# Performance work log

Hardware: AMD Instinct MI355X
Metric: run time of the kernel (lower is better)

The kernel has to match this reference:

```python
import jax, jax.numpy as jnp
import numpy as np

EPS = 1e-12

def _fuzzy_laplacian_weights(theta, src, dst, num_nodes):
    # Continuous edge directions: forward (src->dst) strength cos^2(theta),
    # backward (dst->src) strength sin^2(theta); each symmetrically normalized
    # by its own weighted in/out degrees.
    c = jnp.cos(theta); s = jnp.sin(theta)
    w_f = c * c
    w_b = s * s
    def norm(w):
        deg_out = jax.ops.segment_sum(w, src, num_segments=num_nodes)
        deg_in = jax.ops.segment_sum(w, dst, num_segments=num_nodes)
        return w * jax.lax.rsqrt(deg_out[src] * deg_in[dst] + EPS)
    return norm(w_f), norm(w_b)

def setup_inputs() -> dict:
    key = jax.random.key(0)
    ks = jax.random.split(key, 12)
    N, E, D, H, O, L = 50000, 800000, 128, 128, 64, 2
    x = jax.random.normal(ks[0], (N, D), dtype=jnp.float32)
    edge_index = jax.random.randint(ks[1], (2, E), 0, N, dtype=jnp.int64)
    theta = jax.random.uniform(ks[2], (E,), dtype=jnp.float32) * (np.pi / 2)
    sc = 0.05
    Ws2d = jax.random.normal(ks[3], (L, D, H), dtype=jnp.float32) * sc
    Wd2s = jax.random.normal(ks[4], (L, D, H), dtype=jnp.float32) * sc
    Wself = jax.random.normal(ks[5], (L, D, H), dtype=jnp.float32) * sc
    bs2d = jnp.zeros((L, H), jnp.float32)
    bd2s = jnp.zeros((L, H), jnp.float32)
    bself = jnp.zeros((L, H), jnp.float32)
    W_ro = jax.random.normal(ks[6], (H, O), dtype=jnp.float32) * sc
    b_ro = jnp.zeros((O,), jnp.float32)
    return {"x": x, "edge_index": edge_index, "theta": theta,
            "Ws2d": Ws2d, "Wd2s": Wd2s, "Wself": Wself,
            "bs2d": bs2d, "bd2s": bd2s, "bself": bself,
            "W_ro": W_ro, "b_ro": b_ro}

def reference(x, edge_index, theta, Ws2d, Wd2s, Wself, bs2d, bd2s, bself, W_ro, b_ro):
    N = x.shape[0]
    src, dst = edge_index[0], edge_index[1]
    w_f, w_b = _fuzzy_laplacian_weights(theta, src, dst, N)
    L = Ws2d.shape[0]
    for i in range(L):
        xj = x[src]                               # [E, D] gather
        a_s2d = jax.ops.segment_sum(xj * w_f[:, None], dst, num_segments=N)
        a_d2s = jax.ops.segment_sum(xj * w_b[:, None], dst, num_segments=N)
        h = (a_s2d @ Ws2d[i] + bs2d[i]
             + a_d2s @ Wd2s[i] + bd2s[i]
             + x @ Wself[i] + bself[i])
        if i != L - 1:
            h = jax.nn.relu(h)
            h = h / jnp.maximum(jnp.linalg.norm(h, axis=1, keepdims=True), EPS)
        x = h
    return x @ W_ro + b_ro
```

## Files before the change

kernel.cpp:

```cpp
#include <hip/hip_runtime.h>
#include <math.h>


constexpr int D = 128;
typedef unsigned long long u64;
typedef __attribute__((ext_vector_type(8))) short bf16x8;
typedef __attribute__((ext_vector_type(4))) float f32x4;

__device__ __forceinline__ u64 pack_wc(float f) {
    return (1ULL << 44) | (u64)(f * 16777216.0f + 0.5f);
}
__device__ __forceinline__ void unpack_wc(u64 p, float& sumf, float& cnt) {
    cnt  = (float)(unsigned)(p >> 44);
    sumf = (float)(p & ((1ULL << 44) - 1)) * (1.0f / 16777216.0f);
}

__device__ __forceinline__ void split_bf16(float x, short& hi, short& lo) {
    unsigned xb = __float_as_uint(x);
    hi = (short)(xb >> 16);
    float h = __uint_as_float(xb & 0xffff0000u);
    lo = (short)(__float_as_uint(x - h) >> 16);
}

__global__ __launch_bounds__(256) void edge_wdeg_kernel(
    const float* __restrict__ theta, const int* __restrict__ src, const int* __restrict__ dst,
    u64* __restrict__ packed_out, u64* __restrict__ packed_in, int E)
{
    int e = blockIdx.x * 256 + threadIdx.x;
    if (e >= E) return;
    float c = cosf(theta[e]);
    u64 p = pack_wc(c * c);
    atomicAdd(&packed_out[src[e]], p);
    atomicAdd(&packed_in[dst[e]], p);
}

__global__ __launch_bounds__(1024) void scan_kernel(
    const u64* __restrict__ packed_in, int* __restrict__ startv, int N)
{
    __shared__ int wsum[16];
    __shared__ int carry;
    if (threadIdx.x == 0) carry = 0;
    __syncthreads();
    const int lane = threadIdx.x & 63, wid = threadIdx.x >> 6;
    for (int base = 0; base < N; base += 2048) {
        int i0 = base + threadIdx.x * 2;
        int i1 = i0 + 1;
        int v0 = (i0 < N) ? (int)(packed_in[i0] >> 44) : 0;
        int v1 = (i1 < N) ? (int)(packed_in[i1] >> 44) : 0;
        int pair = v0 + v1;
        int x = pair;
        #pragma unroll
        for (int d = 1; d < 64; d <<= 1) {
            int t = __shfl_up(x, d);
            if (lane >= d) x += t;
        }
        if (lane == 63) wsum[wid] = x;
        __syncthreads();
        if (wid == 0) {
            int s = (lane < 16) ? wsum[lane] : 0;
            #pragma unroll
            for (int d = 1; d < 16; d <<= 1) {
                int t = __shfl_up(s, d);
                if (lane >= d) s += t;
            }
            if (lane < 16) wsum[lane] = s;
        }
        __syncthreads();
        int woff = (wid == 0) ? 0 : wsum[wid - 1];
        int excl = carry + woff + x - pair;
        if (i0 < N) startv[i0] = excl;
        if (i1 < N) startv[i1] = excl + v0;
        __syncthreads();
        if (threadIdx.x == 1023) carry += wsum[15];
        __syncthreads();
    }
}

__global__ __launch_bounds__(256) void scatter_kernel(
    const float* __restrict__ theta, const int* __restrict__ src, const int* __restrict__ dst,
    const u64* __restrict__ packed_out, const u64* __restrict__ packed_in,
    int* __restrict__ startv, int4* __restrict__ s_edge, int E)
{
    int e = blockIdx.x * 256 + threadIdx.x;
    if (e >= E) return;
    int u = src[e], v = dst[e];
    float s, c;
    sincosf(theta[e], &s, &c);
    float f = c * c, b = s * s;
    float fo, co, fi, ci;
    unpack_wc(packed_out[u], fo, co);
    unpack_wc(packed_in[v], fi, ci);
    float bo = co - fo, bi = ci - fi;
    f *= rsqrtf(fo * fi + 1e-12f);
    b *= rsqrtf(bo * bi + 1e-12f);
    int pos = atomicAdd(&startv[v], 1);
    s_edge[pos] = make_int4(u, __float_as_int(f), __float_as_int(b), 0);
}

__global__ __launch_bounds__(256) void wpack_kernel(
    const float* __restrict__ W1, const float* __restrict__ W2, const float* __restrict__ W3,
    short* __restrict__ wp)
{
    int idx = blockIdx.x * 256 + threadIdx.x;
    if (idx >= 3 * 8 * 4 * 64) return;
    int lane = idx & 63;
    int t = (idx >> 6) & 3;
    int c = (idx >> 8) & 7;
    int m = idx >> 11;
    const float* W = (m == 0) ? W1 : ((m == 1) ? W2 : W3);
    int col  = c * 16 + (lane & 15);
    int row0 = t * 32 + (lane >> 4) * 8;
    short hi[8], lo[8];
    #pragma unroll
    for (int j = 0; j < 8; ++j)
        split_bf16(W[(size_t)(row0 + j) * 128 + col], hi[j], lo[j]);
    short* dst = wp + (size_t)idx * 16;
    #pragma unroll
    for (int j = 0; j < 8; ++j) { dst[j] = hi[j]; dst[8 + j] = lo[j]; }
}

__global__ __launch_bounds__(256) void wpack_ro_kernel(
    const float* __restrict__ W, short* __restrict__ wp)
{
    int idx = blockIdx.x * 256 + threadIdx.x;
    if (idx >= 4 * 4 * 64) return;
    int lane = idx & 63;
    int t = (idx >> 6) & 3;
    int c = idx >> 8;
    int col  = c * 16 + (lane & 15);
    int row0 = t * 32 + (lane >> 4) * 8;
    short hi[8], lo[8];
    #pragma unroll
    for (int j = 0; j < 8; ++j)
        split_bf16(W[(size_t)(row0 + j) * 64 + col], hi[j], lo[j]);
    short* dst = wp + (size_t)idx * 16;
    #pragma unroll
    for (int j = 0; j < 8; ++j) { dst[j] = hi[j]; dst[8 + j] = lo[j]; }
}

__global__ __launch_bounds__(256) void agg_x_kernel(
    const int* __restrict__ endv, const int4* __restrict__ s_edge,
    const float* __restrict__ x,
    float* __restrict__ a1, float* __restrict__ a2, int N)
{
    int v = blockIdx.x * 4 + (threadIdx.x >> 6);
    if (v >= N) return;
    int lane = threadIdx.x & 63;
    int beg = (v == 0) ? 0 : endv[v - 1];
    int end = endv[v];
    float2 s1 = make_float2(0.f, 0.f), s2 = make_float2(0.f, 0.f);
    int e = beg;
    for (; e + 3 < end; e += 4) {
        int4 E0 = s_edge[e], E1 = s_edge[e + 1], E2 = s_edge[e + 2], E3 = s_edge[e + 3];
        float2 x0 = reinterpret_cast<const float2*>(x + (size_t)E0.x * 128)[lane];
        float2 x1 = reinterpret_cast<const float2*>(x + (size_t)E1.x * 128)[lane];
        float2 x2 = reinterpret_cast<const float2*>(x + (size_t)E2.x * 128)[lane];
        float2 x3 = reinterpret_cast<const float2*>(x + (size_t)E3.x * 128)[lane];
        float f0 = __int_as_float(E0.y), b0 = __int_as_float(E0.z);
        float f1 = __int_as_float(E1.y), b1 = __int_as_float(E1.z);
        float f2 = __int_as_float(E2.y), b2 = __int_as_float(E2.z);
        float f3 = __int_as_float(E3.y), b3 = __int_as_float(E3.z);
        s1.x = fmaf(f0, x0.x, s1.x); s1.y = fmaf(f0, x0.y, s1.y);
        s2.x = fmaf(b0, x0.x, s2.x); s2.y = fmaf(b0, x0.y, s2.y);
        s1.x = fmaf(f1, x1.x, s1.x); s1.y = fmaf(f1, x1.y, s1.y);
        s2.x = fmaf(b1, x1.x, s2.x); s2.y = fmaf(b1, x1.y, s2.y);
        s1.x = fmaf(f2, x2.x, s1.x); s1.y = fmaf(f2, x2.y, s1.y);
        s2.x = fmaf(b2, x2.x, s2.x); s2.y = fmaf(b2, x2.y, s2.y);
        s1.x = fmaf(f3, x3.x, s1.x); s1.y = fmaf(f3, x3.y, s1.y);
        s2.x = fmaf(b3, x3.x, s2.x); s2.y = fmaf(b3, x3.y, s2.y);
    }
    for (; e < end; ++e) {
        int4 E0 = s_edge[e];
        float f0 = __int_as_float(E0.y), b0 = __int_as_float(E0.z);
        float2 x0 = reinterpret_cast<const float2*>(x + (size_t)E0.x * 128)[lane];
        s1.x = fmaf(f0, x0.x, s1.x); s1.y = fmaf(f0, x0.y, s1.y);
        s2.x = fmaf(b0, x0.x, s2.x); s2.y = fmaf(b0, x0.y, s2.y);
    }
    reinterpret_cast<float2*>(a1 + (size_t)v * 128)[lane] = s1;
    reinterpret_cast<float2*>(a2 + (size_t)v * 128)[lane] = s2;
}

template <bool NORM>
__global__ __launch_bounds__(256, 2) void matmul_fused_kernel(
    const float* __restrict__ a1, const float* __restrict__ a2,
    const float* __restrict__ xin, const short* __restrict__ wp,
    const float* __restrict__ b1, const float* __restrict__ b2, const float* __restrict__ b3,
    float* __restrict__ h, int N)
{
    const int lane = threadIdx.x & 63, wid = threadIdx.x >> 6;
    const int row0 = blockIdx.x * 64 + wid * 16;

    int arow = row0 + (lane & 15);
    if (arow >= N) arow = N - 1;
    const size_t roff = (size_t)arow * 128 + (lane >> 4) * 8;
    const float* srcs[3] = {a1, a2, xin};
    bf16x8 ahi[3][4], alo[3][4];
    #pragma unroll
    for (int m = 0; m < 3; ++m) {
        const float* rp = srcs[m] + roff;
        #pragma unroll
        for (int t = 0; t < 4; ++t) {
            float4 v0 = *reinterpret_cast<const float4*>(rp + t * 32);
            float4 v1 = *reinterpret_cast<const float4*>(rp + t * 32 + 4);
            float f[8] = {v0.x, v0.y, v0.z, v0.w, v1.x, v1.y, v1.z, v1.w};
            #pragma unroll
            for (int j = 0; j < 8; ++j) {
                short hh, ll;
                split_bf16(f[j], hh, ll);
                ahi[m][t][j] = hh;
                alo[m][t][j] = ll;
            }
        }
    }

    const int colbase = lane & 15;
    const int rbase = row0 + (lane >> 4) * 4;
    f32x4 acc[8];
    #pragma unroll
    for (int c = 0; c < 8; ++c) {
        f32x4 a = {0.f, 0.f, 0.f, 0.f};
        #pragma unroll
        for (int t = 0; t < 4; ++t) {
            #pragma unroll
            for (int m = 0; m < 3; ++m) {
                const short* bp = wp + (size_t)((m * 8 + c) * 4 + t) * 1024 + lane * 16;
                bf16x8 bhi = *reinterpret_cast<const bf16x8*>(bp);
                bf16x8 blo = *reinterpret_cast<const bf16x8*>(bp + 8);
                a = __builtin_amdgcn_mfma_f32_16x16x32_bf16(ahi[m][t], bhi, a, 0, 0, 0);
                a = __builtin_amdgcn_mfma_f32_16x16x32_bf16(ahi[m][t], blo, a, 0, 0, 0);
                a = __builtin_amdgcn_mfma_f32_16x16x32_bf16(alo[m][t], bhi, a, 0, 0, 0);
            }
        }
        int col = c * 16 + colbase;
        float bias = b1[col] + b2[col] + b3[col];
        a[0] += bias; a[1] += bias; a[2] += bias; a[3] += bias;
        acc[c] = a;
    }

    if (NORM) {
        #pragma unroll
        for (int c = 0; c < 8; ++c) {
            acc[c][0] = fmaxf(acc[c][0], 0.f);
            acc[c][1] = fmaxf(acc[c][1], 0.f);
            acc[c][2] = fmaxf(acc[c][2], 0.f);
            acc[c][3] = fmaxf(acc[c][3], 0.f);
        }
        float ss[4] = {0.f, 0.f, 0.f, 0.f};
        #pragma unroll
        for (int c = 0; c < 8; ++c) {
            ss[0] = fmaf(acc[c][0], acc[c][0], ss[0]);
            ss[1] = fmaf(acc[c][1], acc[c][1], ss[1]);
            ss[2] = fmaf(acc[c][2], acc[c][2], ss[2]);
            ss[3] = fmaf(acc[c][3], acc[c][3], ss[3]);
        }
        #pragma unroll
        for (int r = 0; r < 4; ++r) {
            #pragma unroll
            for (int m = 1; m < 16; m <<= 1) ss[r] += __shfl_xor(ss[r], m);
        }
        float sc[4];
        #pragma unroll
        for (int r = 0; r < 4; ++r) sc[r] = 1.f / fmaxf(sqrtf(ss[r]), 1e-12f);
        #pragma unroll
        for (int c = 0; c < 8; ++c) {
            acc[c][0] *= sc[0]; acc[c][1] *= sc[1];
            acc[c][2] *= sc[2]; acc[c][3] *= sc[3];
        }
    }

    #pragma unroll
    for (int c = 0; c < 8; ++c) {
        int col = c * 16 + colbase;
        #pragma unroll
        for (int r = 0; r < 4; ++r) {
            int rr = rbase + r;
            if (rr < N) h[(size_t)rr * 128 + col] = acc[c][r];
        }
    }
}

__global__ __launch_bounds__(256, 2) void readout_mfma_kernel(
    const float* __restrict__ xin, const short* __restrict__ wp,
    const float* __restrict__ bias, float* __restrict__ out, int N)
{
    const int lane = threadIdx.x & 63, wid = threadIdx.x >> 6;
    const int row0 = blockIdx.x * 64 + wid * 16;

    int arow = row0 + (lane & 15);
    if (arow >= N) arow = N - 1;
    const float* rp = xin + (size_t)arow * 128 + (lane >> 4) * 8;
    bf16x8 ahi[4], alo[4];
    #pragma unroll
    for (int t = 0; t < 4; ++t) {
        float4 v0 = *reinterpret_cast<const float4*>(rp + t * 32);
        float4 v1 = *reinterpret_cast<const float4*>(rp + t * 32 + 4);
        float f[8] = {v0.x, v0.y, v0.z, v0.w, v1.x, v1.y, v1.z, v1.w};
        #pragma unroll
        for (int j = 0; j < 8; ++j) {
            short hh, ll;
            split_bf16(f[j], hh, ll);
            ahi[t][j] = hh;
            alo[t][j] = ll;
        }
    }

    const int colbase = lane & 15;
    const int rbase = row0 + (lane >> 4) * 4;
    #pragma unroll
    for (int c = 0; c < 4; ++c) {
        f32x4 a = {0.f, 0.f, 0.f, 0.f};
        #pragma unroll
        for (int t = 0; t < 4; ++t) {
            const short* bp = wp + (size_t)((c * 4 + t) * 64 + lane) * 16;
            bf16x8 bhi = *reinterpret_cast<const bf16x8*>(bp);
            bf16x8 blo = *reinterpret_cast<const bf16x8*>(bp + 8);
            a = __builtin_amdgcn_mfma_f32_16x16x32_bf16(ahi[t], bhi, a, 0, 0, 0);
            a = __builtin_amdgcn_mfma_f32_16x16x32_bf16(ahi[t], blo, a, 0, 0, 0);
            a = __builtin_amdgcn_mfma_f32_16x16x32_bf16(alo[t], bhi, a, 0, 0, 0);
        }
        int col = c * 16 + colbase;
        float bv = bias[col];
        a[0] += bv; a[1] += bv; a[2] += bv; a[3] += bv;
        #pragma unroll
        for (int r = 0; r < 4; ++r) {
            int rr = rbase + r;
            if (rr < N) out[(size_t)rr * 64 + col] = a[r];
        }
    }
}

extern "C" void kernel_launch(void* const* d_in, const int* in_sizes, int n_in,
                              void* d_out, int out_size, void* d_ws, size_t ws_size,
                              hipStream_t stream)
{
    const float* x     = (const float*)d_in[0];
    const int*   ei    = (const int*)d_in[1];
    const float* theta = (const float*)d_in[2];
    const float* Ws2d  = (const float*)d_in[3];
    const float* Wd2s  = (const float*)d_in[4];
    const float* Wself = (const float*)d_in[5];
    const float* bs2d  = (const float*)d_in[6];
    const float* bd2s  = (const float*)d_in[7];
    const float* bself = (const float*)d_in[8];
    const float* W_ro  = (const float*)d_in[9];
    const float* b_ro  = (const float*)d_in[10];
    float* out = (float*)d_out;

    const int N = in_sizes[0] / D;
    const int E = in_sizes[2];
    const int L = in_sizes[3] / (D * D);

    const int* src = ei;
    const int* dst = ei + E;

    u64*  packed_out = (u64*)d_ws;
    u64*  packed_in  = packed_out + N;
    int*  startv     = (int*)(packed_in + N);
    int4* s_edge     = (int4*)(startv + N);
    short* wpack     = (short*)(s_edge + E);
    short* wpack_ro  = wpack + (size_t)L * 98304;
    float* a1   = (float*)(wpack_ro + 16384);
    float* a2   = a1 + (size_t)N * D;
    float* accA = a2 + (size_t)N * D;
    float* accB = accA + (size_t)N * D;

    hipMemsetAsync(packed_out, 0, (size_t)2 * N * sizeof(u64), stream);
    edge_wdeg_kernel<<<(E + 255) / 256, 256, 0, stream>>>(
        theta, src, dst, packed_out, packed_in, E);
    scan_kernel<<<1, 1024, 0, stream>>>(packed_in, startv, N);
    scatter_kernel<<<(E + 255) / 256, 256, 0, stream>>>(
        theta, src, dst, packed_out, packed_in, startv, s_edge, E);
    for (int i = 0; i < L; ++i)
        wpack_kernel<<<(6144 + 255) / 256, 256, 0, stream>>>(
            Ws2d + (size_t)i * D * D, Wd2s + (size_t)i * D * D, Wself + (size_t)i * D * D,
            wpack + (size_t)i * 98304);
    wpack_ro_kernel<<<4, 256, 0, stream>>>(W_ro, wpack_ro);

    const float* xin = x;
    float* accs[2] = {accA, accB};
    for (int i = 0; i < L; ++i) {
        float* acc = accs[i & 1];
        agg_x_kernel<<<(N + 3) / 4, 256, 0, stream>>>(
            startv, s_edge, xin, a1, a2, N);
        if (i != L - 1)
            matmul_fused_kernel<true><<<(N + 63) / 64, 256, 0, stream>>>(
                a1, a2, xin, wpack + (size_t)i * 98304,
                bs2d + (size_t)i * D, bd2s + (size_t)i * D, bself + (size_t)i * D,
                acc, N);
        else
            matmul_fused_kernel<false><<<(N + 63) / 64, 256, 0, stream>>>(
                a1, a2, xin, wpack + (size_t)i * 98304,
                bs2d + (size_t)i * D, bd2s + (size_t)i * D, bself + (size_t)i * D,
                acc, N);
        xin = acc;
    }
    readout_mfma_kernel<<<(N + 63) / 64, 256, 0, stream>>>(xin, wpack_ro, b_ro, out, N);
}
```

Measured before the change: 498.2 us.

## Fuse readout into last matmul, factor degree norm, merge weight packing

The readout matmul now runs inside the final layer's fused matmul kernel. The layer output is staged through shared memory and fed to MFMA against the packed readout weights, so the hidden state is never written to or read back from global memory. The per-edge normalization rsqrt(deg_out*deg_in) is split into a per-source factor applied in scatter and a per-destination factor applied once per node after aggregation. This removes the random packed_in gather per edge. Weight packing for all layers and the readout becomes one launch. Costs are extra shared memory per block and a changed epsilon handling at zero degree.

```diff
diff --git a/kernel.cpp b/kernel.cpp
--- a/kernel.cpp
+++ b/kernel.cpp
@@ -78,7 +78,7 @@
 
 __global__ __launch_bounds__(256) void scatter_kernel(
     const float* __restrict__ theta, const int* __restrict__ src, const int* __restrict__ dst,
-    const u64* __restrict__ packed_out, const u64* __restrict__ packed_in,
+    const u64* __restrict__ packed_out,
     int* __restrict__ startv, int4* __restrict__ s_edge, int E)
 {
     int e = blockIdx.x * 256 + threadIdx.x;
@@ -86,61 +86,59 @@
     int u = src[e], v = dst[e];
     float s, c;
     sincosf(theta[e], &s, &c);
-    float f = c * c, b = s * s;
-    float fo, co, fi, ci;
+    float fo, co;
     unpack_wc(packed_out[u], fo, co);
-    unpack_wc(packed_in[v], fi, ci);
-    float bo = co - fo, bi = ci - fi;
-    f *= rsqrtf(fo * fi + 1e-12f);
-    b *= rsqrtf(bo * bi + 1e-12f);
+    float bo = co - fo;
+    float f = c * c * (fo > 0.f ? rsqrtf(fo) : 0.f);
+    float b = s * s * (bo > 0.f ? rsqrtf(bo) : 0.f);
     int pos = atomicAdd(&startv[v], 1);
     s_edge[pos] = make_int4(u, __float_as_int(f), __float_as_int(b), 0);
 }
 
-__global__ __launch_bounds__(256) void wpack_kernel(
-    const float* __restrict__ W1, const float* __restrict__ W2, const float* __restrict__ W3,
-    short* __restrict__ wp)
+__global__ __launch_bounds__(256) void wpack_all_kernel(
+    const float* __restrict__ Ws2d, const float* __restrict__ Wd2s,
+    const float* __restrict__ Wself, const float* __restrict__ W_ro,
+    short* __restrict__ wp, short* __restrict__ wp_ro, int L)
 {
     int idx = blockIdx.x * 256 + threadIdx.x;
-    if (idx >= 3 * 8 * 4 * 64) return;
-    int lane = idx & 63;
-    int t = (idx >> 6) & 3;
-    int c = (idx >> 8) & 7;
-    int m = idx >> 11;
-    const float* W = (m == 0) ? W1 : ((m == 1) ? W2 : W3);
-    int col  = c * 16 + (lane & 15);
-    int row0 = t * 32 + (lane >> 4) * 8;
-    short hi[8], lo[8];
-    #pragma unroll
-    for (int j = 0; j < 8; ++j)
-        split_bf16(W[(size_t)(row0 + j) * 128 + col], hi[j], lo[j]);
-    short* dst = wp + (size_t)idx * 16;
-    #pragma unroll
-    for (int j = 0; j < 8; ++j) { dst[j] = hi[j]; dst[8 + j] = lo[j]; }
-}
-
-__global__ __launch_bounds__(256) void wpack_ro_kernel(
-    const float* __restrict__ W, short* __restrict__ wp)
-{
-    int idx = blockIdx.x * 256 + threadIdx.x;
-    if (idx >= 4 * 4 * 64) return;
-    int lane = idx & 63;
-    int t = (idx >> 6) & 3;
-    int c = idx >> 8;
-    int col  = c * 16 + (lane & 15);
-    int row0 = t * 32 + (lane >> 4) * 8;
-    short hi[8], lo[8];
-    #pragma unroll
-    for (int j = 0; j < 8; ++j)
-        split_bf16(W[(size_t)(row0 + j) * 64 + col], hi[j], lo[j]);
-    short* dst = wp + (size_t)idx * 16;
-    #pragma unroll
-    for (int j = 0; j < 8; ++j) { dst[j] = hi[j]; dst[8 + j] = lo[j]; }
+    int layerTotal = L * 6144;
+    if (idx < layerTotal) {
+        int layer = idx / 6144;
+        int r = idx - layer * 6144;
+        int lane = r & 63;
+        int t = (r >> 6) & 3;
+        int c = (r >> 8) & 7;
+        int m = r >> 11;
+        const float* W = ((m == 0) ? Ws2d : ((m == 1) ? Wd2s : Wself)) + (size_t)layer * D * D;
+        int col  = c * 16 + (lane & 15);
+        int row0 = t * 32 + (lane >> 4) * 8;
+        short* dst = wp + (size_t)layer * 98304 + (size_t)r * 16;
+        #pragma unroll
+        for (int j = 0; j < 8; ++j) {
+            short hi, lo;
+            split_bf16(W[(size_t)(row0 + j) * 128 + col], hi, lo);
+            dst[j] = hi; dst[8 + j] = lo;
+        }
+    } else if (idx < layerTotal + 1024) {
+        int r = idx - layerTotal;
+        int lane = r & 63;
+        int t = (r >> 6) & 3;
+        int c = r >> 8;
+        int col  = c * 16 + (lane & 15);
+        int row0 = t * 32 + (lane >> 4) * 8;
+        short* dst = wp_ro + (size_t)r * 16;
+        #pragma unroll
+        for (int j = 0; j < 8; ++j) {
+            short hi, lo;
+            split_bf16(W_ro[(size_t)(row0 + j) * 64 + col], hi, lo);
+            dst[j] = hi; dst[8 + j] = lo;
+        }
+    }
 }
 
 __global__ __launch_bounds__(256) void agg_x_kernel(
     const int* __restrict__ endv, const int4* __restrict__ s_edge,
-    const float* __restrict__ x,
+    const u64* __restrict__ packed_in, const float* __restrict__ x,
     float* __restrict__ a1, float* __restrict__ a2, int N)
 {
     int v = blockIdx.x * 4 + (threadIdx.x >> 6);
@@ -176,17 +174,26 @@
         s1.x = fmaf(f0, x0.x, s1.x); s1.y = fmaf(f0, x0.y, s1.y);
         s2.x = fmaf(b0, x0.x, s2.x); s2.y = fmaf(b0, x0.y, s2.y);
     }
+    float fi, ci;
+    unpack_wc(packed_in[v], fi, ci);
+    float bi = ci - fi;
+    float pif = fi > 0.f ? rsqrtf(fi) : 0.f;
+    float pib = bi > 0.f ? rsqrtf(bi) : 0.f;
+    s1.x *= pif; s1.y *= pif;
+    s2.x *= pib; s2.y *= pib;
     reinterpret_cast<float2*>(a1 + (size_t)v * 128)[lane] = s1;
     reinterpret_cast<float2*>(a2 + (size_t)v * 128)[lane] = s2;
 }
 
-template <bool NORM>
+template <bool NORM, bool RO>
 __global__ __launch_bounds__(256, 2) void matmul_fused_kernel(
     const float* __restrict__ a1, const float* __restrict__ a2,
     const float* __restrict__ xin, const short* __restrict__ wp,
     const float* __restrict__ b1, const float* __restrict__ b2, const float* __restrict__ b3,
-    float* __restrict__ h, int N)
-{
+    const short* __restrict__ wp_ro, const float* __restrict__ b_ro,
+    float* __restrict__ h, float* __restrict__ out, int N)
+{
+    __shared__ float ls[4][16 * 132];
     const int lane = threadIdx.x & 63, wid = threadIdx.x >> 6;
     const int row0 = blockIdx.x * 64 + wid * 16;
 
@@ -268,63 +275,60 @@
         }
     }
 
-    #pragma unroll
-    for (int c = 0; c < 8; ++c) {
-        int col = c * 16 + colbase;
-        #pragma unroll
-        for (int r = 0; r < 4; ++r) {
-            int rr = rbase + r;
-            if (rr < N) h[(size_t)rr * 128 + col] = acc[c][r];
-        }
-    }
-}
-
-__global__ __launch_bounds__(256, 2) void readout_mfma_kernel(
-    const float* __restrict__ xin, const short* __restrict__ wp,
-    const float* __restrict__ bias, float* __restrict__ out, int N)
-{
-    const int lane = threadIdx.x & 63, wid = threadIdx.x >> 6;
-    const int row0 = blockIdx.x * 64 + wid * 16;
-
-    int arow = row0 + (lane & 15);
-    if (arow >= N) arow = N - 1;
-    const float* rp = xin + (size_t)arow * 128 + (lane >> 4) * 8;
-    bf16x8 ahi[4], alo[4];
-    #pragma unroll
-    for (int t = 0; t < 4; ++t) {
-        float4 v0 = *reinterpret_cast<const float4*>(rp + t * 32);
-        float4 v1 = *reinterpret_cast<const float4*>(rp + t * 32 + 4);
-        float f[8] = {v0.x, v0.y, v0.z, v0.w, v1.x, v1.y, v1.z, v1.w};
-        #pragma unroll
-        for (int j = 0; j < 8; ++j) {
-            short hh, ll;
-            split_bf16(f[j], hh, ll);
-            ahi[t][j] = hh;
-            alo[t][j] = ll;
-        }
-    }
-
-    const int colbase = lane & 15;
-    const int rbase = row0 + (lane >> 4) * 4;
-    #pragma unroll
-    for (int c = 0; c < 4; ++c) {
-        f32x4 a = {0.f, 0.f, 0.f, 0.f};
+    if (!RO) {
+        #pragma unroll
+        for (int c = 0; c < 8; ++c) {
+            int col = c * 16 + colbase;
+            #pragma unroll
+            for (int r = 0; r < 4; ++r) {
+                int rr = rbase + r;
+                if (rr < N) h[(size_t)rr * 128 + col] = acc[c][r];
+            }
+        }
+    } else {
+        #pragma unroll
+        for (int c = 0; c < 8; ++c) {
+            int col = c * 16 + colbase;
+            #pragma unroll
+            for (int r = 0; r < 4; ++r)
+                ls[wid][((lane >> 4) * 4 + r) * 132 + col] = acc[c][r];
+        }
+        __syncthreads();
+        const float* lrow = &ls[wid][(lane & 15) * 132 + (lane >> 4) * 8];
+        bf16x8 hhi[4], hlo[4];
         #pragma unroll
         for (int t = 0; t < 4; ++t) {
-            const short* bp = wp + (size_t)((c * 4 + t) * 64 + lane) * 16;
-            bf16x8 bhi = *reinterpret_cast<const bf16x8*>(bp);
-            bf16x8 blo = *reinterpret_cast<const bf16x8*>(bp + 8);
-            a = __builtin_amdgcn_mfma_f32_16x16x32_bf16(ahi[t], bhi, a, 0, 0, 0);
-            a = __builtin_amdgcn_mfma_f32_16x16x32_bf16(ahi[t], blo, a, 0, 0, 0);
-            a = __builtin_amdgcn_mfma_f32_16x16x32_bf16(alo[t], bhi, a, 0, 0, 0);
-        }
-        int col = c * 16 + colbase;
-        float bv = bias[col];
-        a[0] += bv; a[1] += bv; a[2] += bv; a[3] += bv;
-        #pragma unroll
-        for (int r = 0; r < 4; ++r) {
-            int rr = rbase + r;
-            if (rr < N) out[(size_t)rr * 64 + col] = a[r];
+            float4 v0 = *reinterpret_cast<const float4*>(lrow + t * 32);
+            float4 v1 = *reinterpret_cast<const float4*>(lrow + t * 32 + 4);
+            float f[8] = {v0.x, v0.y, v0.z, v0.w, v1.x, v1.y, v1.z, v1.w};
+            #pragma unroll
+            for (int j = 0; j < 8; ++j) {
+                short hh, ll;
+                split_bf16(f[j], hh, ll);
+                hhi[t][j] = hh;
+                hlo[t][j] = ll;
+            }
+        }
+        #pragma unroll
+        for (int c2 = 0; c2 < 4; ++c2) {
+            f32x4 a = {0.f, 0.f, 0.f, 0.f};
+            #pragma unroll
+            for (int t = 0; t < 4; ++t) {
+                const short* bp = wp_ro + (size_t)((c2 * 4 + t) * 64 + lane) * 16;
+                bf16x8 bhi = *reinterpret_cast<const bf16x8*>(bp);
+                bf16x8 blo = *reinterpret_cast<const bf16x8*>(bp + 8);
+                a = __builtin_amdgcn_mfma_f32_16x16x32_bf16(hhi[t], bhi, a, 0, 0, 0);
+                a = __builtin_amdgcn_mfma_f32_16x16x32_bf16(hhi[t], blo, a, 0, 0, 0);
+                a = __builtin_amdgcn_mfma_f32_16x16x32_bf16(hlo[t], bhi, a, 0, 0, 0);
+            }
+            int col = c2 * 16 + colbase;
+            float bv = b_ro[col];
+            a[0] += bv; a[1] += bv; a[2] += bv; a[3] += bv;
+            #pragma unroll
+            for (int r = 0; r < 4; ++r) {
+                int rr = rbase + r;
+                if (rr < N) out[(size_t)rr * 64 + col] = a[r];
+            }
         }
     }
 }
@@ -369,30 +373,26 @@
         theta, src, dst, packed_out, packed_in, E);
     scan_kernel<<<1, 1024, 0, stream>>>(packed_in, startv, N);
     scatter_kernel<<<(E + 255) / 256, 256, 0, stream>>>(
-        theta, src, dst, packed_out, packed_in, startv, s_edge, E);
-    for (int i = 0; i < L; ++i)
-        wpack_kernel<<<(6144 + 255) / 256, 256, 0, stream>>>(
-            Ws2d + (size_t)i * D * D, Wd2s + (size_t)i * D * D, Wself + (size_t)i * D * D,
-            wpack + (size_t)i * 98304);
-    wpack_ro_kernel<<<4, 256, 0, stream>>>(W_ro, wpack_ro);
+        theta, src, dst, packed_out, startv, s_edge, E);
+    wpack_all_kernel<<<(L * 6144 + 1024 + 255) / 256, 256, 0, stream>>>(
+        Ws2d, Wd2s, Wself, W_ro, wpack, wpack_ro, L);
 
     const float* xin = x;
     float* accs[2] = {accA, accB};
     for (int i = 0; i < L; ++i) {
         float* acc = accs[i & 1];
         agg_x_kernel<<<(N + 3) / 4, 256, 0, stream>>>(
-            startv, s_edge, xin, a1, a2, N);
+            startv, s_edge, packed_in, xin, a1, a2, N);
         if (i != L - 1)
-            matmul_fused_kernel<true><<<(N + 63) / 64, 256, 0, stream>>>(
+            matmul_fused_kernel<true, false><<<(N + 63) / 64, 256, 0, stream>>>(
                 a1, a2, xin, wpack + (size_t)i * 98304,
                 bs2d + (size_t)i * D, bd2s + (size_t)i * D, bself + (size_t)i * D,
-                acc, N);
+                wpack_ro, b_ro, acc, out, N);
         else
-            matmul_fused_kernel<false><<<(N + 63) / 64, 256, 0, stream>>>(
+            matmul_fused_kernel<false, true><<<(N + 63) / 64, 256, 0, stream>>>(
                 a1, a2, xin, wpack + (size_t)i * 98304,
                 bs2d + (size_t)i * D, bd2s + (size_t)i * D, bself + (size_t)i * D,
-                acc, N);
+                wpack_ro, b_ro, acc, out, N);
         xin = acc;
     }
-    readout_mfma_kernel<<<(N + 63) / 64, 256, 0, stream>>>(xin, wpack_ro, b_ro, out, N);
-}
+}
```

Result: faster. 483.7 us (-2.9%).
